# Performance work log

Measured on AMD Instinct MI355X. Metric: run time of the kernel, lower is better.

Reference implementation:

```python
import jax, jax.numpy as jnp
import numpy as np
from jax import lax

B, CIN, H, W = 2, 512, 64, 64
CD = CIN // 2            # down_dim = 256
CQ = CD // 8             # q/k channels = 32
EPS = 1e-5               # BatchNorm eps


def _conv3(x, w, b):
    # 3x3 conv, stride 1, padding 1 (init padding=1), NCHW/OIHW
    y = lax.conv_general_dilated(x, w, (1, 1), [(1, 1), (1, 1)],
                                 dimension_numbers=('NCHW', 'OIHW', 'NCHW'))
    return y + b[None, :, None, None]


def _bn(x, g, b, m, v):
    scale = g / jnp.sqrt(v + EPS)
    return x * scale[None, :, None, None] + (b - m * scale)[None, :, None, None]


def _prelu(x, a):
    return jnp.where(x > 0, x, a * x)


def _p1(x, w, b):
    # 1x1 conv as channel matmul
    return jnp.einsum('bchw,oc->bohw', x, w) + b[None, :, None, None]


def setup_inputs() -> dict:
    key = jax.random.key(0)
    it = iter(jax.random.split(key, 64))
    def nrm(shape, s=0.05):
        return jax.random.normal(next(it), shape, jnp.float32) * s
    inp = {
        'input_rgb': jax.random.normal(next(it), (B, CIN, H, W), jnp.float32),
        'input_dsm': jax.random.normal(next(it), (B, CIN, H, W), jnp.float32),
    }
    for m in ('rgb', 'dsm'):
        inp['conv_w_' + m] = nrm((CD, CIN, 3, 3))
        inp['conv_b_' + m] = nrm((CD,))
        inp['bn_g_' + m] = 1.0 + nrm((CD,))
        inp['bn_b_' + m] = nrm((CD,))
        inp['bn_m_' + m] = nrm((CD,))
        inp['bn_v_' + m] = jax.random.uniform(next(it), (CD,), jnp.float32, 0.5, 1.5)
        inp['prelu_' + m] = jnp.float32(0.25)
        inp['q_w_' + m] = nrm((CQ, CD)); inp['q_b_' + m] = nrm((CQ,))
        inp['k_w_' + m] = nrm((CQ, CD)); inp['k_b_' + m] = nrm((CQ,))
        inp['v_w_' + m] = nrm((CD, CD)); inp['v_b_' + m] = nrm((CD,))
        inp['up_w_' + m] = nrm((CIN, CD)); inp['up_b_' + m] = nrm((CIN,))
        inp['gamma_' + m] = jnp.float32(0.1)  # learned residual gate (zero-init in torch)
    return inp


def reference(input_rgb, input_dsm,
              conv_w_rgb, conv_b_rgb, bn_g_rgb, bn_b_rgb, bn_m_rgb, bn_v_rgb, prelu_rgb,
              q_w_rgb, q_b_rgb, k_w_rgb, k_b_rgb, v_w_rgb, v_b_rgb, up_w_rgb, up_b_rgb, gamma_rgb,
              conv_w_dsm, conv_b_dsm, bn_g_dsm, bn_b_dsm, bn_m_dsm, bn_v_dsm, prelu_dsm,
              q_w_dsm, q_b_dsm, k_w_dsm, k_b_dsm, v_w_dsm, v_b_dsm, up_w_dsm, up_b_dsm, gamma_dsm):
    conv_rgb = _prelu(_bn(_conv3(input_rgb, conv_w_rgb, conv_b_rgb),
                          bn_g_rgb, bn_b_rgb, bn_m_rgb, bn_v_rgb), prelu_rgb)
    conv_dsm = _prelu(_bn(_conv3(input_dsm, conv_w_dsm, conv_b_dsm),
                          bn_g_dsm, bn_b_dsm, bn_m_dsm, bn_v_dsm), prelu_dsm)
    b, c, h, w = conv_rgb.shape
    n = h * w
    q_rgb = _p1(conv_rgb, q_w_rgb, q_b_rgb).reshape(b, CQ, n)
    k_rgb = _p1(conv_rgb, k_w_rgb, k_b_rgb).reshape(b, CQ, n)
    v_rgb = _p1(conv_rgb, v_w_rgb, v_b_rgb).reshape(b, c, n)
    q_dsm = _p1(conv_dsm, q_w_dsm, q_b_dsm).reshape(b, CQ, n)
    k_dsm = _p1(conv_dsm, k_w_dsm, k_b_dsm).reshape(b, CQ, n)
    v_dsm = _p1(conv_dsm, v_w_dsm, v_b_dsm).reshape(b, c, n)
    # cross-modal unscaled attention: dsm queries attend over rgb keys
    attn_rgb = jax.nn.softmax(jnp.einsum('bqn,bqm->bnm', q_dsm, k_rgb), axis=-1)  # [b,n,n]
    o_rgb = jnp.einsum('bcj,bij->bci', v_rgb, attn_rgb).reshape(b, c, h, w)
    o_rgb = gamma_rgb * o_rgb + conv_rgb
    attn_dsm = jax.nn.softmax(jnp.einsum('bqn,bqm->bnm', q_rgb, k_dsm), axis=-1)
    o_dsm = jnp.einsum('bcj,bij->bci', v_dsm, attn_dsm).reshape(b, c, h, w)
    o_dsm = gamma_dsm * o_dsm + conv_dsm
    out_rgb = _p1(o_rgb, up_w_rgb, up_b_rgb) + input_rgb
    out_dsm = _p1(o_dsm, up_w_dsm, up_b_dsm) + input_dsm
    return (out_rgb, out_dsm)
```

## Files before the change

### kernel.cpp

```cpp
#include <hip/hip_runtime.h>
#include <hip/hip_bf16.h>
#include <stdint.h>


constexpr int CINCH = 512;
constexpr int NPIX  = 4096;

typedef __bf16 bf16x8 __attribute__((ext_vector_type(8)));
typedef __bf16 bf16x4 __attribute__((ext_vector_type(4)));
typedef float  f32x4  __attribute__((ext_vector_type(4)));

__device__ __forceinline__ __bf16 f2b(float f) {
    __hip_bfloat16 h = __float2bfloat16(f);
    return *reinterpret_cast<__bf16*>(&h);
}

__device__ __forceinline__ void load_lds16(const void* g, void* l) {
    __builtin_amdgcn_global_load_lds(
        (const __attribute__((address_space(1))) unsigned int*)(uintptr_t)g,
        (__attribute__((address_space(3))) unsigned int*)(uintptr_t)l,
        16, 0, 0);
}

__global__ __launch_bounds__(256)
void prep_w(const float* __restrict__ w_r, const float* __restrict__ w_d,
            const float* __restrict__ cb_r, const float* __restrict__ bg_r,
            const float* __restrict__ bb_r, const float* __restrict__ bm_r,
            const float* __restrict__ bv_r,
            const float* __restrict__ cb_d, const float* __restrict__ bg_d,
            const float* __restrict__ bb_d, const float* __restrict__ bm_d,
            const float* __restrict__ bv_d,
            __bf16* __restrict__ Wt, float* __restrict__ scA,
            float* __restrict__ shB, __bf16* __restrict__ zrow)
{
    const int t = threadIdx.x;
    const int blk = blockIdx.x;
    if (blk < 2304) {
        int gid = blk * 1024 + t * 4;
        int mod = gid >= 1179648;
        int o2  = gid - mod * 1179648;
        int tap = o2 >> 17;
        int r   = o2 & 131071;
        int oc  = r >> 9;
        int ic  = r & 511;
        const float* wsrc = mod ? w_d : w_r;
        long base = ((long)(oc * 512 + ic)) * 9 + tap;
        bf16x4 v;
        v.x = f2b(wsrc[base]);
        v.y = f2b(wsrc[base + 9]);
        v.z = f2b(wsrc[base + 18]);
        v.w = f2b(wsrc[base + 27]);
        *(bf16x4*)&Wt[gid] = v;
    } else if (blk == 2304) {
        unsigned short* z = (unsigned short*)zrow;
        z[t] = 0; z[t + 256] = 0;
    } else {
        int mod = blk - 2305;
        const float* cb = mod ? cb_d : cb_r;
        const float* bg = mod ? bg_d : bg_r;
        const float* bb = mod ? bb_d : bb_r;
        const float* bm = mod ? bm_d : bm_r;
        const float* bv = mod ? bv_d : bv_r;
        int oc = t;
        float sc = bg[oc] * rsqrtf(bv[oc] + 1e-5f);
        scA[mod * 256 + oc] = sc;
        shB[mod * 256 + oc] = (cb[oc] - bm[oc]) * sc + bb[oc];
    }
}

__global__ __launch_bounds__(256)
void prep_gw(const float* __restrict__ qw_r, const float* __restrict__ qw_d,
             const float* __restrict__ kw_r, const float* __restrict__ kw_d,
             const float* __restrict__ vw_r, const float* __restrict__ vw_d,
             const float* __restrict__ uw_r, const float* __restrict__ uw_d,
             __bf16* __restrict__ Wq, __bf16* __restrict__ Wk,
             __bf16* __restrict__ Wv, __bf16* __restrict__ Wu)
{
    int gid = blockIdx.x * 1024 + threadIdx.x * 4;
    __bf16* dst;
    float4 f = make_float4(0.f, 0.f, 0.f, 0.f);
    if (gid < 65536) {
        int mod = gid >> 15, e = gid & 32767;
        dst = Wq + gid;
        if (e < 8192) f = *(const float4*)((mod ? qw_d : qw_r) + e);
    } else if (gid < 131072) {
        int g = gid - 65536;
        int mod = g >> 15, e = g & 32767;
        dst = Wk + g;
        if (e < 8192) f = *(const float4*)((mod ? kw_d : kw_r) + e);
    } else if (gid < 262144) {
        int g = gid - 131072;
        int mod = g >> 16, e = g & 65535;
        dst = Wv + g;
        f = *(const float4*)((mod ? vw_d : vw_r) + e);
    } else {
        int g = gid - 262144;
        int mod = g >> 17, e = g & 131071;
        dst = Wu + g;
        f = *(const float4*)((mod ? uw_d : uw_r) + e);
    }
    bf16x4 o; o.x = f2b(f.x); o.y = f2b(f.y); o.z = f2b(f.z); o.w = f2b(f.w);
    *(bf16x4*)dst = o;
}

__global__ __launch_bounds__(256)
void xpose(const float* __restrict__ inr, const float* __restrict__ ind,
           __bf16* __restrict__ Xp)
{
    __shared__ float tile[32][33];
    const int t = threadIdx.x;
    const int p0 = blockIdx.x * 32;
    const int ic0 = blockIdx.y * 32;
    const int mb = blockIdx.z;
    const int mod = mb >> 1, b = mb & 1;
    const float* src = (mod ? ind : inr) + (long)b * CINCH * NPIX;

    int i = t >> 3, j4 = (t & 7) * 4;
    float4 v = *(const float4*)&src[(long)(ic0 + i) * NPIX + p0 + j4];
    tile[i][j4 + 0] = v.x; tile[i][j4 + 1] = v.y;
    tile[i][j4 + 2] = v.z; tile[i][j4 + 3] = v.w;
    __syncthreads();
    int j = t >> 3, i4 = (t & 7) * 4;
    bf16x4 o;
    o.x = f2b(tile[i4 + 0][j]);
    o.y = f2b(tile[i4 + 1][j]);
    o.z = f2b(tile[i4 + 2][j]);
    o.w = f2b(tile[i4 + 3][j]);
    *(bf16x4*)&Xp[((long)mb * NPIX + p0 + j) * 512 + ic0 + i4] = o;
}

__global__ __launch_bounds__(256)
void t256(const float* __restrict__ src, __bf16* __restrict__ dst)
{
    __shared__ float tile[32][33];
    const int t = threadIdx.x;
    const int p0 = blockIdx.x * 32;
    const int c0 = blockIdx.y * 32;
    const int mb = blockIdx.z;
    const float* s = src + (long)mb * 256 * NPIX;
    __bf16* d = dst + (long)mb * NPIX * 256;

    int i = t >> 3, j4 = (t & 7) * 4;
    float4 v = *(const float4*)&s[(long)(c0 + i) * NPIX + p0 + j4];
    tile[i][j4 + 0] = v.x; tile[i][j4 + 1] = v.y;
    tile[i][j4 + 2] = v.z; tile[i][j4 + 3] = v.w;
    __syncthreads();
    int j = t >> 3, i4 = (t & 7) * 4;
    bf16x4 o;
    o.x = f2b(tile[i4 + 0][j]); o.y = f2b(tile[i4 + 1][j]);
    o.z = f2b(tile[i4 + 2][j]); o.w = f2b(tile[i4 + 3][j]);
    *(bf16x4*)&d[((long)(p0 + j)) * 256 + c0 + i4] = o;
}

__global__ __launch_bounds__(256)
void conv_mfma(const __bf16* __restrict__ Wt, const __bf16* __restrict__ Xp,
               const __bf16* __restrict__ zrow, const float* __restrict__ scA,
               const float* __restrict__ shB, const float* __restrict__ prr,
               const float* __restrict__ prd, float* __restrict__ conv)
{
    __shared__ __bf16 As[64 * 32];
    __shared__ __bf16 Bs[128 * 32];

    const int t = threadIdx.x;
    const int n0 = blockIdx.x * 128;
    const int m0 = blockIdx.y * 64;
    const int mb = blockIdx.z;
    const int mod = mb >> 1;

    const __bf16* Am = Wt + (long)mod * 9 * 256 * 512;
    const __bf16* Xb = Xp + (long)mb * NPIX * 512;

    const int rowa = t >> 2;
    const int c16  = t & 3;
    char* ldsA  = (char*)As + (t >> 6) * 1024;
    char* ldsB0 = (char*)Bs + (t >> 6) * 1024;
    char* ldsB1 = ldsB0 + 4096;

    const int lane = t & 63, quad = lane >> 4, l15 = lane & 15, w = t >> 6;
    const int nw0 = w * 32;
    const char* abase = (const char*)As + l15 * 64 + quad * 16;
    const char* bbase = (const char*)Bs + (nw0 + l15) * 64 + quad * 16;

    f32x4 acc[4][2];
#pragma unroll
    for (int i = 0; i < 4; ++i)
#pragma unroll
        for (int j = 0; j < 2; ++j) acc[i][j] = (f32x4)0.f;

    for (int tap = 0; tap < 9; ++tap) {
        const int dy = tap / 3 - 1, dx = tap % 3 - 1;
        const __bf16* srcA = Am + (long)tap * 131072 + (long)(m0 + rowa) * 512 + c16 * 8;
        const __bf16* srcB0; const __bf16* srcB1;
        bool v0, v1;
        {
            int n = n0 + rowa;
            int x = n & 63, y = n >> 6;
            v0 = !((dx == -1 && x == 0) || (dx == 1 && x == 63) ||
                   (dy == -1 && y == 0) || (dy == 1 && y == 63));
            srcB0 = v0 ? (Xb + (long)(n + dy * 64 + dx) * 512 + c16 * 8)
                       : (zrow + c16 * 8);
            n += 64; x = n & 63; y = n >> 6;
            v1 = !((dx == -1 && x == 0) || (dx == 1 && x == 63) ||
                   (dy == -1 && y == 0) || (dy == 1 && y == 63));
            srcB1 = v1 ? (Xb + (long)(n + dy * 64 + dx) * 512 + c16 * 8)
                       : (zrow + c16 * 8);
        }

        for (int ic0 = 0; ic0 < 512; ic0 += 32) {
            load_lds16(srcA + ic0, ldsA);
            load_lds16(srcB0 + (v0 ? ic0 : 0), ldsB0);
            load_lds16(srcB1 + (v1 ? ic0 : 0), ldsB1);
            __syncthreads();

            bf16x8 af[4], bfr[2];
#pragma unroll
            for (int i = 0; i < 4; ++i) af[i]  = *(const bf16x8*)(abase + i * 1024);
#pragma unroll
            for (int j = 0; j < 2; ++j) bfr[j] = *(const bf16x8*)(bbase + j * 1024);
#pragma unroll
            for (int i = 0; i < 4; ++i)
#pragma unroll
                for (int j = 0; j < 2; ++j)
                    acc[i][j] = __builtin_amdgcn_mfma_f32_16x16x32_bf16(
                        af[i], bfr[j], acc[i][j], 0, 0, 0);
            __syncthreads();
        }
    }

    const float alpha = (mod ? prd : prr)[0];
    float* outp = conv + (long)mb * 256 * NPIX;
#pragma unroll
    for (int i = 0; i < 4; ++i) {
#pragma unroll
        for (int r = 0; r < 4; ++r) {
            int oc = m0 + 16 * i + quad * 4 + r;
            float sc = scA[mod * 256 + oc];
            float sh = shB[mod * 256 + oc];
            float* orow = outp + (long)oc * NPIX;
#pragma unroll
            for (int j = 0; j < 2; ++j) {
                int n = n0 + nw0 + 16 * j + l15;
                float y = acc[i][j][r] * sc + sh;
                y = (y > 0.f) ? y : alpha * y;
                orow[n] = y;
            }
        }
    }
}

__global__ __launch_bounds__(256)
void proj_mfma(const __bf16* __restrict__ Wb, int mstride,
               const __bf16* __restrict__ Bt,
               const float* __restrict__ bias_r, const float* __restrict__ bias_d,
               __bf16* __restrict__ dstT, __bf16* __restrict__ dstV,
               float* __restrict__ dstU,
               const float* __restrict__ resid_r, const float* __restrict__ resid_d,
               int mode)
{
    __shared__ __bf16 As[128 * 32];
    __shared__ __bf16 Bs[128 * 32];

    const int t = threadIdx.x;
    const int n0 = blockIdx.x * 128;
    const int m0 = blockIdx.y * 128;
    const int mb = blockIdx.z;
    const int mod = mb >> 1, b = mb & 1;

    const __bf16* Am = Wb + (long)mod * mstride;
    const __bf16* Bm = Bt + (long)mb * (NPIX * 256);
    const float* bias = mod ? bias_d : bias_r;

    const int rowa = t >> 2, c16 = t & 3;
    char* ldsA0 = (char*)As + (t >> 6) * 1024;
    char* ldsA1 = ldsA0 + 4096;
    char* ldsB0 = (char*)Bs + (t >> 6) * 1024;
    char* ldsB1 = ldsB0 + 4096;
    const __bf16* srcA = Am + (long)(m0 + rowa) * 256 + c16 * 8;
    const __bf16* srcB = Bm + (long)(n0 + rowa) * 256 + c16 * 8;

    const int lane = t & 63, quad = lane >> 4, l15 = lane & 15, w = t >> 6;
    const int mw = (w >> 1) * 64, nw = (w & 1) * 64;
    const char* abase = (const char*)As + (mw + l15) * 64 + quad * 16;
    const char* bbase = (const char*)Bs + (nw + l15) * 64 + quad * 16;

    f32x4 acc[4][4];
#pragma unroll
    for (int i = 0; i < 4; ++i)
#pragma unroll
        for (int j = 0; j < 4; ++j) acc[i][j] = (f32x4)0.f;

    for (int kc = 0; kc < 256; kc += 32) {
        load_lds16(srcA + kc, ldsA0);
        load_lds16(srcA + kc + 16384, ldsA1);
        load_lds16(srcB + kc, ldsB0);
        load_lds16(srcB + kc + 16384, ldsB1);
        __syncthreads();

        bf16x8 af[4], bfr[4];
#pragma unroll
        for (int i = 0; i < 4; ++i) af[i]  = *(const bf16x8*)(abase + i * 1024);
#pragma unroll
        for (int j = 0; j < 4; ++j) bfr[j] = *(const bf16x8*)(bbase + j * 1024);
#pragma unroll
        for (int i = 0; i < 4; ++i)
#pragma unroll
            for (int j = 0; j < 4; ++j)
                acc[i][j] = __builtin_amdgcn_mfma_f32_16x16x32_bf16(
                    af[i], bfr[j], acc[i][j], 0, 0, 0);
        __syncthreads();
    }

    if (mode == 0) {
        if (mw == 0) {
            __bf16* dbase = dstT + (long)mb * (NPIX * 32);
#pragma unroll
            for (int fi = 0; fi < 2; ++fi)
#pragma unroll
                for (int r = 0; r < 4; ++r) {
                    int oc = 16 * fi + quad * 4 + r;
                    float bi = bias[oc];
#pragma unroll
                    for (int fj = 0; fj < 4; ++fj) {
                        int n = n0 + nw + 16 * fj + l15;
                        dbase[(long)n * 32 + oc] = f2b(acc[fi][fj][r] + bi);
                    }
                }
        }
    } else if (mode == 1) {
        __bf16* dv = dstV + (long)mb * (256 * NPIX);
#pragma unroll
        for (int fi = 0; fi < 4; ++fi)
#pragma unroll
            for (int r = 0; r < 4; ++r) {
                int c = m0 + mw + 16 * fi + quad * 4 + r;
                float bi = bias[c];
                __bf16* row = dv + (long)c * NPIX;
#pragma unroll
                for (int fj = 0; fj < 4; ++fj) {
                    int n = n0 + nw + 16 * fj + l15;
                    row[n] = f2b(acc[fi][fj][r] + bi);
                }
            }
    } else {
        float* du = dstU + (long)mod * 4194304 + (long)b * 2097152;
        const float* rs = (mod ? resid_d : resid_r) + (long)b * 2097152;
#pragma unroll
        for (int fi = 0; fi < 4; ++fi)
#pragma unroll
            for (int r = 0; r < 4; ++r) {
                int oc = m0 + mw + 16 * fi + quad * 4 + r;
                float bi = bias[oc];
                const float* rrow = rs + (long)oc * NPIX;
                float* orow = du + (long)oc * NPIX;
#pragma unroll
                for (int fj = 0; fj < 4; ++fj) {
                    int n = n0 + nw + 16 * fj + l15;
                    orow[n] = acc[fi][fj][r] + bi + rrow[n];
                }
            }
    }
}

__global__ __launch_bounds__(256)
void attn_stats_mfma(const __bf16* __restrict__ Qt, const __bf16* __restrict__ Kt,
                     float* __restrict__ rmp, float* __restrict__ rlp)
{
    __shared__ __bf16 Qs[128 * 32];
    __shared__ __bf16 Ks[128 * 32];
    __shared__ float red[2][128];
    __shared__ float mfin[128];

    const int t  = threadIdx.x;
    const int i0 = blockIdx.x * 128;
    const int mbo = blockIdx.y;
    const int o  = mbo >> 1, b = mbo & 1;
    const int seg = blockIdx.z;
    const int jbase = seg * 2048;
    const int mbK = o * 2 + b, mbQ = (1 - o) * 2 + b;

    const __bf16* Qg = Qt + (long)mbQ * 131072;
    const __bf16* Kg = Kt + (long)mbK * 131072;

    const int lane = t & 63, quad = lane >> 4, l15 = lane & 15, w = t >> 6;
    const int mS = (w >> 1) * 64;
    const int nS = (w & 1) * 64;

    load_lds16((const char*)Qg + (long)i0 * 64 + t * 16, (char*)Qs + (t >> 6) * 1024);
    load_lds16((const char*)Qg + (long)i0 * 64 + 4096 + t * 16,
               (char*)Qs + 4096 + (t >> 6) * 1024);
    __syncthreads();

    bf16x8 qa[4];
#pragma unroll
    for (int fi = 0; fi < 4; ++fi)
        qa[fi] = *(const bf16x8*)((const char*)Qs + (mS + 16 * fi + l15) * 64 + quad * 16);

    const f32x4 zero4 = (f32x4)0.f;
    float mloc[16];
#pragma unroll
    for (int e = 0; e < 16; ++e) mloc[e] = -3.0e38f;

    for (int j0 = jbase; j0 < jbase + 2048; j0 += 128) {
        __syncthreads();
        load_lds16((const char*)Kg + (long)j0 * 64 + t * 16, (char*)Ks + (t >> 6) * 1024);
        load_lds16((const char*)Kg + (long)j0 * 64 + 4096 + t * 16,
                   (char*)Ks + 4096 + (t >> 6) * 1024);
        __syncthreads();
#pragma unroll
        for (int fj = 0; fj < 4; ++fj) {
            bf16x8 kb = *(const bf16x8*)((const char*)Ks + (nS + 16 * fj + l15) * 64 + quad * 16);
#pragma unroll
            for (int fi = 0; fi < 4; ++fi) {
                f32x4 s = __builtin_amdgcn_mfma_f32_16x16x32_bf16(qa[fi], kb, zero4, 0, 0, 0);
#pragma unroll
                for (int r = 0; r < 4; ++r)
                    mloc[fi * 4 + r] = fmaxf(mloc[fi * 4 + r], s[r]);
            }
        }
    }
#pragma unroll
    for (int d = 1; d < 16; d <<= 1)
#pragma unroll
        for (int e = 0; e < 16; ++e)
            mloc[e] = fmaxf(mloc[e], __shfl_xor(mloc[e], d, 64));
    if (l15 == 0) {
#pragma unroll
        for (int fi = 0; fi < 4; ++fi)
#pragma unroll
            for (int r = 0; r < 4; ++r)
                red[w & 1][mS + 16 * fi + quad * 4 + r] = mloc[fi * 4 + r];
    }
    __syncthreads();
    if (t < 128) mfin[t] = fmaxf(red[0][t], red[1][t]);
    __syncthreads();

    float mi[16];
#pragma unroll
    for (int fi = 0; fi < 4; ++fi)
#pragma unroll
        for (int r = 0; r < 4; ++r)
            mi[fi * 4 + r] = mfin[mS + 16 * fi + quad * 4 + r];
    float sloc[16];
#pragma unroll
    for (int e = 0; e < 16; ++e) sloc[e] = 0.f;

    for (int j0 = jbase; j0 < jbase + 2048; j0 += 128) {
        __syncthreads();
        load_lds16((const char*)Kg + (long)j0 * 64 + t * 16, (char*)Ks + (t >> 6) * 1024);
        load_lds16((const char*)Kg + (long)j0 * 64 + 4096 + t * 16,
                   (char*)Ks + 4096 + (t >> 6) * 1024);
        __syncthreads();
#pragma unroll
        for (int fj = 0; fj < 4; ++fj) {
            bf16x8 kb = *(const bf16x8*)((const char*)Ks + (nS + 16 * fj + l15) * 64 + quad * 16);
#pragma unroll
            for (int fi = 0; fi < 4; ++fi) {
                f32x4 s = __builtin_amdgcn_mfma_f32_16x16x32_bf16(qa[fi], kb, zero4, 0, 0, 0);
#pragma unroll
                for (int r = 0; r < 4; ++r)
                    sloc[fi * 4 + r] += __expf(s[r] - mi[fi * 4 + r]);
            }
        }
    }
#pragma unroll
    for (int d = 1; d < 16; d <<= 1)
#pragma unroll
        for (int e = 0; e < 16; ++e)
            sloc[e] += __shfl_xor(sloc[e], d, 64);
    if (l15 == 0) {
#pragma unroll
        for (int fi = 0; fi < 4; ++fi)
#pragma unroll
            for (int r = 0; r < 4; ++r)
                red[w & 1][mS + 16 * fi + quad * 4 + r] = sloc[fi * 4 + r];
    }
    __syncthreads();
    if (t < 128) {
        rmp[seg * 16384 + mbo * 4096 + i0 + t] = mfin[t];
        rlp[seg * 16384 + mbo * 4096 + i0 + t] = red[0][t] + red[1][t];
    }
}

__global__ __launch_bounds__(256)
void stats_merge(const float* __restrict__ rmp, const float* __restrict__ rlp,
                 float* __restrict__ rmb, float* __restrict__ rlb)
{
    int idx = blockIdx.x * 256 + threadIdx.x;
    float m0 = rmp[idx], m1 = rmp[16384 + idx];
    float l0 = rlp[idx], l1 = rlp[16384 + idx];
    float m = fmaxf(m0, m1);
    float l = l0 * __expf(m0 - m) + l1 * __expf(m1 - m);
    rmb[idx] = m;
    rlb[idx] = 1.f / l;
}

__global__ __launch_bounds__(256)
void attn_pv_mfma(const __bf16* __restrict__ Qt, const __bf16* __restrict__ Kt,
                  const __bf16* __restrict__ Vb,
                  float* __restrict__ part0, float* __restrict__ part1,
                  const float* __restrict__ rmb, const float* __restrict__ rlb)
{
    __shared__ __bf16 Qs[128 * 32];
    __shared__ __bf16 Ks[64 * 32];
    __shared__ __bf16 Vs[2 * 128 * 32];
    __shared__ __bf16 Ps[2 * 128 * 32];

    const int t  = threadIdx.x;
    const int i0 = blockIdx.x * 128;
    const int c0 = blockIdx.y * 128;
    const int zb = blockIdx.z;
    const int seg = zb >> 2, mb = zb & 3;
    const int o  = mb >> 1, b = mb & 1;
    const int mbK = mb, mbQ = (1 - o) * 2 + b;
    const int jbase = seg * 2048;

    const __bf16* Qg = Qt + (long)mbQ * 131072;
    const __bf16* Kg = Kt + (long)mbK * 131072;
    const __bf16* Vg = Vb + (long)mbK * 1048576;
    const float* rm = rmb + mb * 4096;
    const float* rl = rlb + mb * 4096;

    const int lane = t & 63, quad = lane >> 4, l15 = lane & 15, w = t >> 6;
    const int mw = (w >> 1) * 64;
    const int nw = (w & 1) * 64;
    const int mS = (w >> 1) * 64;
    const int nS = (w & 1) * 32;
    const int ksP = w & 1;

    load_lds16((const char*)Qg + (long)i0 * 64 + t * 16, (char*)Qs + (t >> 6) * 1024);
    load_lds16((const char*)Qg + (long)i0 * 64 + 4096 + t * 16,
               (char*)Qs + 4096 + (t >> 6) * 1024);

    float mlv[16], rlv[16];
#pragma unroll
    for (int fi = 0; fi < 4; ++fi)
#pragma unroll
        for (int r = 0; r < 4; ++r) {
            int i = i0 + mS + 16 * fi + quad * 4 + r;
            mlv[fi * 4 + r] = rm[i];
            rlv[fi * 4 + r] = rl[i];
        }

    f32x4 acc[4][4];
#pragma unroll
    for (int i = 0; i < 4; ++i)
#pragma unroll
        for (int j = 0; j < 4; ++j) acc[i][j] = (f32x4)0.f;
    const f32x4 zero4 = (f32x4)0.f;

    for (int j0 = jbase; j0 < jbase + 2048; j0 += 64) {
        __syncthreads();
        load_lds16((const char*)Kg + (long)j0 * 64 + t * 16, (char*)Ks + (t >> 6) * 1024);
#pragma unroll
        for (int ii = 0; ii < 4; ++ii) {
            int s = ii * 256 + t;
            int ks = s >> 9, cc = (s >> 2) & 127, blk = s & 3;
            load_lds16((const char*)Vg + (long)(c0 + cc) * 8192 + (j0 + ks * 32) * 2 + blk * 16,
                       (char*)Vs + ii * 4096 + (t >> 6) * 1024);
        }
        __syncthreads();

        bf16x8 qa[4], kb2[2];
#pragma unroll
        for (int fi = 0; fi < 4; ++fi)
            qa[fi] = *(const bf16x8*)((const char*)Qs + (mS + 16 * fi + l15) * 64 + quad * 16);
#pragma unroll
        for (int fj = 0; fj < 2; ++fj)
            kb2[fj] = *(const bf16x8*)((const char*)Ks + (nS + 16 * fj + l15) * 64 + quad * 16);
        f32x4 sA[4][2];
#pragma unroll
        for (int fi = 0; fi < 4; ++fi)
#pragma unroll
            for (int fj = 0; fj < 2; ++fj)
                sA[fi][fj] = __builtin_amdgcn_mfma_f32_16x16x32_bf16(
                    qa[fi], kb2[fj], zero4, 0, 0, 0);

        __bf16* prow = Ps + ksP * 4096;
#pragma unroll
        for (int fi = 0; fi < 4; ++fi)
#pragma unroll
            for (int fj = 0; fj < 2; ++fj) {
                int jl = 16 * fj + l15;
#pragma unroll
                for (int r = 0; r < 4; ++r) {
                    float p = __expf(sA[fi][fj][r] - mlv[fi * 4 + r]) * rlv[fi * 4 + r];
                    prow[(mS + 16 * fi + quad * 4 + r) * 32 + jl] = f2b(p);
                }
            }
        __syncthreads();

#pragma unroll
        for (int ks = 0; ks < 2; ++ks) {
            bf16x8 va[4], pb[4];
#pragma unroll
            for (int fi = 0; fi < 4; ++fi)
                va[fi] = *(const bf16x8*)((const char*)Vs + ks * 8192 +
                                          (mw + 16 * fi + l15) * 64 + quad * 16);
#pragma unroll
            for (int fj = 0; fj < 4; ++fj)
                pb[fj] = *(const bf16x8*)((const char*)Ps + ks * 8192 +
                                          (nw + 16 * fj + l15) * 64 + quad * 16);
#pragma unroll
            for (int fi = 0; fi < 4; ++fi)
#pragma unroll
                for (int fj = 0; fj < 4; ++fj)
                    acc[fi][fj] = __builtin_amdgcn_mfma_f32_16x16x32_bf16(
                        va[fi], pb[fj], acc[fi][fj], 0, 0, 0);
        }
    }

    float* pg = (seg ? part1 : part0) + (long)mb * 1048576;
#pragma unroll
    for (int fi = 0; fi < 4; ++fi) {
#pragma unroll
        for (int r = 0; r < 4; ++r) {
            int c = c0 + mw + 16 * fi + quad * 4 + r;
            float* zr = pg + (long)c * 4096;
#pragma unroll
            for (int fj = 0; fj < 4; ++fj) {
                int i = i0 + nw + 16 * fj + l15;
                zr[i] = acc[fi][fj][r];
            }
        }
    }
}

__global__ __launch_bounds__(256)
void zred_t(const float* __restrict__ p0, const float* __restrict__ p1,
            const float* __restrict__ convb, __bf16* __restrict__ Zt,
            const float* __restrict__ g_r, const float* __restrict__ g_d)
{
    __shared__ float tile[32][33];
    const int t = threadIdx.x;
    const int pix0 = blockIdx.x * 32;
    const int c0 = blockIdx.y * 32;
    const int mb = blockIdx.z;
    const int o = mb >> 1;
    const float gamma = (o ? g_d : g_r)[0];
    const long base = (long)mb * 1048576;

    int i = t >> 3, j4 = (t & 7) * 4;
    long row = base + (long)(c0 + i) * 4096 + pix0 + j4;
    float4 a = *(const float4*)&p0[row];
    float4 b = *(const float4*)&p1[row];
    float4 cv = *(const float4*)&convb[row];
    tile[i][j4 + 0] = gamma * (a.x + b.x) + cv.x;
    tile[i][j4 + 1] = gamma * (a.y + b.y) + cv.y;
    tile[i][j4 + 2] = gamma * (a.z + b.z) + cv.z;
    tile[i][j4 + 3] = gamma * (a.w + b.w) + cv.w;
    __syncthreads();
    int j = t >> 3, i4 = (t & 7) * 4;
    bf16x4 oq;
    oq.x = f2b(tile[i4 + 0][j]); oq.y = f2b(tile[i4 + 1][j]);
    oq.z = f2b(tile[i4 + 2][j]); oq.w = f2b(tile[i4 + 3][j]);
    *(bf16x4*)&Zt[(long)mb * NPIX * 256 + (long)(pix0 + j) * 256 + c0 + i4] = oq;
}

extern "C" void kernel_launch(void* const* d_in, const int* in_sizes, int n_in,
                              void* d_out, int out_size, void* d_ws, size_t ws_size,
                              hipStream_t stream)
{
    const float* in_rgb = (const float*)d_in[0];
    const float* in_dsm = (const float*)d_in[1];
    auto P = [&](int i) { return (const float*)d_in[i]; };

    float* ws    = (float*)d_ws;
    float* conv  = ws;
    float* part0 = ws + 4194304;
    float* rmb   = ws + 8388608;
    float* rlb   = ws + 8404992;
    float* rmp   = ws + 8421376;
    float* rlp   = ws + 8454144;
    float* scA   = ws + 8486912;
    float* shB   = ws + 8487424;
    __bf16* zrow = (__bf16*)(ws + 8487936);
    __bf16* Wt   = (__bf16*)(ws + 8488192);
    __bf16* Xp   = (__bf16*)(ws + 9667840);
    float*  part1 = ws + 9667840;
    __bf16* Qt   = (__bf16*)(ws + 13862144);
    __bf16* Kt   = (__bf16*)(ws + 14124288);
    __bf16* Vbb  = (__bf16*)(ws + 14386432);
    __bf16* Ct   = (__bf16*)(ws + 16483584);
    __bf16* Zt   = (__bf16*)(ws + 18580736);
    __bf16* Wq   = (__bf16*)(ws + 20677888);
    __bf16* Wk   = (__bf16*)(ws + 20710656);
    __bf16* Wv   = (__bf16*)(ws + 20743424);
    __bf16* Wu   = (__bf16*)(ws + 20808960);

    prep_w<<<2307, 256, 0, stream>>>(
        P(2), P(18), P(3), P(4), P(5), P(6), P(7),
        P(19), P(20), P(21), P(22), P(23),
        Wt, scA, shB, zrow);
    prep_gw<<<512, 256, 0, stream>>>(
        P(9), P(25), P(11), P(27), P(13), P(29), P(15), P(31),
        Wq, Wk, Wv, Wu);
    xpose<<<dim3(128, 16, 4), 256, 0, stream>>>(in_rgb, in_dsm, Xp);

    conv_mfma<<<dim3(32, 4, 4), 256, 0, stream>>>(
        Wt, Xp, zrow, scA, shB, P(8), P(24), conv);
    t256<<<dim3(128, 8, 4), 256, 0, stream>>>(conv, Ct);

    proj_mfma<<<dim3(32, 1, 4), 256, 0, stream>>>(
        Wq, 32768, Ct, P(10), P(26), Qt, nullptr, nullptr, nullptr, nullptr, 0);
    proj_mfma<<<dim3(32, 1, 4), 256, 0, stream>>>(
        Wk, 32768, Ct, P(12), P(28), Kt, nullptr, nullptr, nullptr, nullptr, 0);
    proj_mfma<<<dim3(32, 2, 4), 256, 0, stream>>>(
        Wv, 65536, Ct, P(14), P(30), nullptr, Vbb, nullptr, nullptr, nullptr, 1);

    attn_stats_mfma<<<dim3(32, 4, 2), 256, 0, stream>>>(Qt, Kt, rmp, rlp);
    stats_merge<<<64, 256, 0, stream>>>(rmp, rlp, rmb, rlb);

    attn_pv_mfma<<<dim3(32, 2, 8), 256, 0, stream>>>(
        Qt, Kt, Vbb, part0, part1, rmb, rlb);

    zred_t<<<dim3(128, 8, 4), 256, 0, stream>>>(
        part0, part1, conv, Zt, P(17), P(33));

    proj_mfma<<<dim3(32, 4, 4), 256, 0, stream>>>(
        Wu, 131072, Zt, P(16), P(32), nullptr, nullptr, (float*)d_out,
        in_rgb, in_dsm, 2);
}
```

Before: 406.0 us.

## Use online softmax stats, exp2 prescaling, and retile attention PV over all channels

Queries are prescaled by log2(e) so every exponential becomes exp2f. The softmax-stats kernel now computes the running max and sum in one pass with online rescaling instead of two passes over K, and it splits keys into four segments that are merged afterwards. The PV kernel now covers all 256 channels per block with 64 query rows, so QK^T and the exponentials are computed once per row rather than once per channel half. It also uses an XOR-swizzled P tile and applies the 1/l normalization at the output. The trade-offs are more exp work per element in the online pass, more registers and LDS for V, and reuse of the part0 buffer for the stats scratch.

```diff
diff --git a/kernel.cpp b/kernel.cpp
--- a/kernel.cpp
+++ b/kernel.cpp
@@ -255,7 +255,7 @@
                __bf16* __restrict__ dstT, __bf16* __restrict__ dstV,
                float* __restrict__ dstU,
                const float* __restrict__ resid_r, const float* __restrict__ resid_d,
-               int mode)
+               int mode, float oscale)
 {
     __shared__ __bf16 As[128 * 32];
     __shared__ __bf16 Bs[128 * 32];
@@ -322,7 +322,7 @@
 #pragma unroll
                     for (int fj = 0; fj < 4; ++fj) {
                         int n = n0 + nw + 16 * fj + l15;
-                        dbase[(long)n * 32 + oc] = f2b(acc[fi][fj][r] + bi);
+                        dbase[(long)n * 32 + oc] = f2b((acc[fi][fj][r] + bi) * oscale);
                     }
                 }
         }
@@ -367,15 +367,15 @@
 {
     __shared__ __bf16 Qs[128 * 32];
     __shared__ __bf16 Ks[128 * 32];
-    __shared__ float red[2][128];
-    __shared__ float mfin[128];
+    __shared__ float redm[2][128];
+    __shared__ float redl[2][128];
 
     const int t  = threadIdx.x;
     const int i0 = blockIdx.x * 128;
     const int mbo = blockIdx.y;
     const int o  = mbo >> 1, b = mbo & 1;
     const int seg = blockIdx.z;
-    const int jbase = seg * 2048;
+    const int jbase = seg * 1024;
     const int mbK = o * 2 + b, mbQ = (1 - o) * 2 + b;
 
     const __bf16* Qg = Qt + (long)mbQ * 131072;
@@ -385,9 +385,9 @@
     const int mS = (w >> 1) * 64;
     const int nS = (w & 1) * 64;
 
-    load_lds16((const char*)Qg + (long)i0 * 64 + t * 16, (char*)Qs + (t >> 6) * 1024);
+    load_lds16((const char*)Qg + (long)i0 * 64 + t * 16, (char*)Qs + w * 1024);
     load_lds16((const char*)Qg + (long)i0 * 64 + 4096 + t * 16,
-               (char*)Qs + 4096 + (t >> 6) * 1024);
+               (char*)Qs + 4096 + w * 1024);
     __syncthreads();
 
     bf16x8 qa[4];
@@ -396,88 +396,67 @@
         qa[fi] = *(const bf16x8*)((const char*)Qs + (mS + 16 * fi + l15) * 64 + quad * 16);
 
     const f32x4 zero4 = (f32x4)0.f;
-    float mloc[16];
-#pragma unroll
-    for (int e = 0; e < 16; ++e) mloc[e] = -3.0e38f;
-
-    for (int j0 = jbase; j0 < jbase + 2048; j0 += 128) {
+    float m_t[16], l_t[16];
+#pragma unroll
+    for (int e = 0; e < 16; ++e) { m_t[e] = -3.0e38f; l_t[e] = 0.f; }
+
+    for (int j0 = jbase; j0 < jbase + 1024; j0 += 128) {
         __syncthreads();
-        load_lds16((const char*)Kg + (long)j0 * 64 + t * 16, (char*)Ks + (t >> 6) * 1024);
+        load_lds16((const char*)Kg + (long)j0 * 64 + t * 16, (char*)Ks + w * 1024);
         load_lds16((const char*)Kg + (long)j0 * 64 + 4096 + t * 16,
-                   (char*)Ks + 4096 + (t >> 6) * 1024);
+                   (char*)Ks + 4096 + w * 1024);
         __syncthreads();
-#pragma unroll
-        for (int fj = 0; fj < 4; ++fj) {
-            bf16x8 kb = *(const bf16x8*)((const char*)Ks + (nS + 16 * fj + l15) * 64 + quad * 16);
-#pragma unroll
-            for (int fi = 0; fi < 4; ++fi) {
-                f32x4 s = __builtin_amdgcn_mfma_f32_16x16x32_bf16(qa[fi], kb, zero4, 0, 0, 0);
-#pragma unroll
-                for (int r = 0; r < 4; ++r)
-                    mloc[fi * 4 + r] = fmaxf(mloc[fi * 4 + r], s[r]);
+
+        bf16x8 kb[4];
+#pragma unroll
+        for (int fj = 0; fj < 4; ++fj)
+            kb[fj] = *(const bf16x8*)((const char*)Ks + (nS + 16 * fj + l15) * 64 + quad * 16);
+#pragma unroll
+        for (int fi = 0; fi < 4; ++fi) {
+            f32x4 sf[4];
+#pragma unroll
+            for (int fj = 0; fj < 4; ++fj)
+                sf[fj] = __builtin_amdgcn_mfma_f32_16x16x32_bf16(qa[fi], kb[fj], zero4, 0, 0, 0);
+#pragma unroll
+            for (int r = 0; r < 4; ++r) {
+                int e = fi * 4 + r;
+                float a = fmaxf(fmaxf(sf[0][r], sf[1][r]), fmaxf(sf[2][r], sf[3][r]));
+                float nm = fmaxf(m_t[e], a);
+                float s = exp2f(sf[0][r] - nm) + exp2f(sf[1][r] - nm)
+                        + exp2f(sf[2][r] - nm) + exp2f(sf[3][r] - nm);
+                l_t[e] = l_t[e] * exp2f(m_t[e] - nm) + s;
+                m_t[e] = nm;
             }
         }
     }
+
 #pragma unroll
     for (int d = 1; d < 16; d <<= 1)
 #pragma unroll
-        for (int e = 0; e < 16; ++e)
-            mloc[e] = fmaxf(mloc[e], __shfl_xor(mloc[e], d, 64));
+        for (int e = 0; e < 16; ++e) {
+            float om = __shfl_xor(m_t[e], d, 64);
+            float ol = __shfl_xor(l_t[e], d, 64);
+            float nm = fmaxf(m_t[e], om);
+            l_t[e] = l_t[e] * exp2f(m_t[e] - nm) + ol * exp2f(om - nm);
+            m_t[e] = nm;
+        }
     if (l15 == 0) {
 #pragma unroll
         for (int fi = 0; fi < 4; ++fi)
 #pragma unroll
-            for (int r = 0; r < 4; ++r)
-                red[w & 1][mS + 16 * fi + quad * 4 + r] = mloc[fi * 4 + r];
-    }
-    __syncthreads();
-    if (t < 128) mfin[t] = fmaxf(red[0][t], red[1][t]);
-    __syncthreads();
-
-    float mi[16];
-#pragma unroll
-    for (int fi = 0; fi < 4; ++fi)
-#pragma unroll
-        for (int r = 0; r < 4; ++r)
-            mi[fi * 4 + r] = mfin[mS + 16 * fi + quad * 4 + r];
-    float sloc[16];
-#pragma unroll
-    for (int e = 0; e < 16; ++e) sloc[e] = 0.f;
-
-    for (int j0 = jbase; j0 < jbase + 2048; j0 += 128) {
-        __syncthreads();
-        load_lds16((const char*)Kg + (long)j0 * 64 + t * 16, (char*)Ks + (t >> 6) * 1024);
-        load_lds16((const char*)Kg + (long)j0 * 64 + 4096 + t * 16,
-                   (char*)Ks + 4096 + (t >> 6) * 1024);
-        __syncthreads();
-#pragma unroll
-        for (int fj = 0; fj < 4; ++fj) {
-            bf16x8 kb = *(const bf16x8*)((const char*)Ks + (nS + 16 * fj + l15) * 64 + quad * 16);
-#pragma unroll
-            for (int fi = 0; fi < 4; ++fi) {
-                f32x4 s = __builtin_amdgcn_mfma_f32_16x16x32_bf16(qa[fi], kb, zero4, 0, 0, 0);
-#pragma unroll
-                for (int r = 0; r < 4; ++r)
-                    sloc[fi * 4 + r] += __expf(s[r] - mi[fi * 4 + r]);
+            for (int r = 0; r < 4; ++r) {
+                redm[w & 1][mS + 16 * fi + quad * 4 + r] = m_t[fi * 4 + r];
+                redl[w & 1][mS + 16 * fi + quad * 4 + r] = l_t[fi * 4 + r];
             }
-        }
-    }
-#pragma unroll
-    for (int d = 1; d < 16; d <<= 1)
-#pragma unroll
-        for (int e = 0; e < 16; ++e)
-            sloc[e] += __shfl_xor(sloc[e], d, 64);
-    if (l15 == 0) {
-#pragma unroll
-        for (int fi = 0; fi < 4; ++fi)
-#pragma unroll
-            for (int r = 0; r < 4; ++r)
-                red[w & 1][mS + 16 * fi + quad * 4 + r] = sloc[fi * 4 + r];
     }
     __syncthreads();
     if (t < 128) {
-        rmp[seg * 16384 + mbo * 4096 + i0 + t] = mfin[t];
-        rlp[seg * 16384 + mbo * 4096 + i0 + t] = red[0][t] + red[1][t];
+        float m0 = redm[0][t], m1 = redm[1][t];
+        float l0 = redl[0][t], l1 = redl[1][t];
+        float m = fmaxf(m0, m1);
+        float l = l0 * exp2f(m0 - m) + l1 * exp2f(m1 - m);
+        rmp[seg * 16384 + mbo * 4096 + i0 + t] = m;
+        rlp[seg * 16384 + mbo * 4096 + i0 + t] = l;
     }
 }
 
@@ -486,10 +465,13 @@
                  float* __restrict__ rmb, float* __restrict__ rlb)
 {
     int idx = blockIdx.x * 256 + threadIdx.x;
-    float m0 = rmp[idx], m1 = rmp[16384 + idx];
-    float l0 = rlp[idx], l1 = rlp[16384 + idx];
-    float m = fmaxf(m0, m1);
-    float l = l0 * __expf(m0 - m) + l1 * __expf(m1 - m);
+    float m = rmp[idx];
+#pragma unroll
+    for (int s = 1; s < 4; ++s) m = fmaxf(m, rmp[s * 16384 + idx]);
+    float l = 0.f;
+#pragma unroll
+    for (int s = 0; s < 4; ++s)
+        l += rlp[s * 16384 + idx] * exp2f(rmp[s * 16384 + idx] - m);
     rmb[idx] = m;
     rlb[idx] = 1.f / l;
 }
@@ -500,16 +482,15 @@
                   float* __restrict__ part0, float* __restrict__ part1,
                   const float* __restrict__ rmb, const float* __restrict__ rlb)
 {
-    __shared__ __bf16 Qs[128 * 32];
+    __shared__ __bf16 Qs[64 * 32];
     __shared__ __bf16 Ks[64 * 32];
-    __shared__ __bf16 Vs[2 * 128 * 32];
-    __shared__ __bf16 Ps[2 * 128 * 32];
+    __shared__ __bf16 Vs[2 * 256 * 32];
+    __shared__ __bf16 Ps[64 * 64];
 
     const int t  = threadIdx.x;
-    const int i0 = blockIdx.x * 128;
-    const int c0 = blockIdx.y * 128;
-    const int zb = blockIdx.z;
-    const int seg = zb >> 2, mb = zb & 3;
+    const int i0 = blockIdx.x * 64;
+    const int seg = blockIdx.y;
+    const int mb = blockIdx.z;
     const int o  = mb >> 1, b = mb & 1;
     const int mbK = mb, mbQ = (1 - o) * 2 + b;
     const int jbase = seg * 2048;
@@ -521,25 +502,16 @@
     const float* rl = rlb + mb * 4096;
 
     const int lane = t & 63, quad = lane >> 4, l15 = lane & 15, w = t >> 6;
-    const int mw = (w >> 1) * 64;
-    const int nw = (w & 1) * 64;
-    const int mS = (w >> 1) * 64;
-    const int nS = (w & 1) * 32;
-    const int ksP = w & 1;
-
-    load_lds16((const char*)Qg + (long)i0 * 64 + t * 16, (char*)Qs + (t >> 6) * 1024);
-    load_lds16((const char*)Qg + (long)i0 * 64 + 4096 + t * 16,
-               (char*)Qs + 4096 + (t >> 6) * 1024);
-
-    float mlv[16], rlv[16];
-#pragma unroll
-    for (int fi = 0; fi < 4; ++fi)
-#pragma unroll
-        for (int r = 0; r < 4; ++r) {
-            int i = i0 + mS + 16 * fi + quad * 4 + r;
-            mlv[fi * 4 + r] = rm[i];
-            rlv[fi * 4 + r] = rl[i];
-        }
+    const int iS = w * 16;
+    const int cw = w * 64;
+
+    load_lds16((const char*)Qg + (long)i0 * 64 + t * 16, (char*)Qs + w * 1024);
+
+    float mlv[4], rlv[4];
+#pragma unroll
+    for (int r = 0; r < 4; ++r) mlv[r] = rm[i0 + iS + quad * 4 + r];
+#pragma unroll
+    for (int fj = 0; fj < 4; ++fj) rlv[fj] = rl[i0 + 16 * fj + l15];
 
     f32x4 acc[4][4];
 #pragma unroll
@@ -548,44 +520,38 @@
         for (int j = 0; j < 4; ++j) acc[i][j] = (f32x4)0.f;
     const f32x4 zero4 = (f32x4)0.f;
 
+    __syncthreads();
+    const bf16x8 qa = *(const bf16x8*)((const char*)Qs + (iS + l15) * 64 + quad * 16);
+
+    const int clv = w * 16 + (lane >> 2);
+    const int jb8 = (lane & 3) * 8;
+
     for (int j0 = jbase; j0 < jbase + 2048; j0 += 64) {
         __syncthreads();
-        load_lds16((const char*)Kg + (long)j0 * 64 + t * 16, (char*)Ks + (t >> 6) * 1024);
-#pragma unroll
-        for (int ii = 0; ii < 4; ++ii) {
-            int s = ii * 256 + t;
-            int ks = s >> 9, cc = (s >> 2) & 127, blk = s & 3;
-            load_lds16((const char*)Vg + (long)(c0 + cc) * 8192 + (j0 + ks * 32) * 2 + blk * 16,
-                       (char*)Vs + ii * 4096 + (t >> 6) * 1024);
-        }
+        load_lds16((const char*)Kg + (long)j0 * 64 + t * 16, (char*)Ks + w * 1024);
         __syncthreads();
 
-        bf16x8 qa[4], kb2[2];
-#pragma unroll
-        for (int fi = 0; fi < 4; ++fi)
-            qa[fi] = *(const bf16x8*)((const char*)Qs + (mS + 16 * fi + l15) * 64 + quad * 16);
-#pragma unroll
-        for (int fj = 0; fj < 2; ++fj)
-            kb2[fj] = *(const bf16x8*)((const char*)Ks + (nS + 16 * fj + l15) * 64 + quad * 16);
-        f32x4 sA[4][2];
-#pragma unroll
-        for (int fi = 0; fi < 4; ++fi)
-#pragma unroll
-            for (int fj = 0; fj < 2; ++fj)
-                sA[fi][fj] = __builtin_amdgcn_mfma_f32_16x16x32_bf16(
-                    qa[fi], kb2[fj], zero4, 0, 0, 0);
-
-        __bf16* prow = Ps + ksP * 4096;
-#pragma unroll
-        for (int fi = 0; fi < 4; ++fi)
-#pragma unroll
-            for (int fj = 0; fj < 2; ++fj) {
-                int jl = 16 * fj + l15;
-#pragma unroll
-                for (int r = 0; r < 4; ++r) {
-                    float p = __expf(sA[fi][fj][r] - mlv[fi * 4 + r]) * rlv[fi * 4 + r];
-                    prow[(mS + 16 * fi + quad * 4 + r) * 32 + jl] = f2b(p);
-                }
+#pragma unroll
+        for (int ii = 0; ii < 8; ++ii) {
+            int ks = ii >> 2;
+            int c = (ii & 3) * 64 + clv;
+            load_lds16((const char*)Vg + (long)c * 8192 + (long)(j0 + ks * 32 + jb8) * 2,
+                       (char*)Vs + ii * 4096 + w * 1024);
+        }
+
+        f32x4 sA[4];
+#pragma unroll
+        for (int fj = 0; fj < 4; ++fj) {
+            bf16x8 kb = *(const bf16x8*)((const char*)Ks + (16 * fj + l15) * 64 + quad * 16);
+            sA[fj] = __builtin_amdgcn_mfma_f32_16x16x32_bf16(qa, kb, zero4, 0, 0, 0);
+        }
+#pragma unroll
+        for (int fj = 0; fj < 4; ++fj)
+#pragma unroll
+            for (int r = 0; r < 4; ++r) {
+                int il = iS + quad * 4 + r;
+                int boff = (il * 128 + (16 * fj + l15) * 2) ^ ((il & 12) << 3);
+                *(__bf16*)((char*)Ps + boff) = f2b(exp2f(sA[fj][r] - mlv[r]));
             }
         __syncthreads();
 
@@ -594,12 +560,14 @@
             bf16x8 va[4], pb[4];
 #pragma unroll
             for (int fi = 0; fi < 4; ++fi)
-                va[fi] = *(const bf16x8*)((const char*)Vs + ks * 8192 +
-                                          (mw + 16 * fi + l15) * 64 + quad * 16);
-#pragma unroll
-            for (int fj = 0; fj < 4; ++fj)
-                pb[fj] = *(const bf16x8*)((const char*)Ps + ks * 8192 +
-                                          (nw + 16 * fj + l15) * 64 + quad * 16);
+                va[fi] = *(const bf16x8*)((const char*)Vs + ks * 16384 +
+                                          (cw + 16 * fi + l15) * 64 + quad * 16);
+#pragma unroll
+            for (int fj = 0; fj < 4; ++fj) {
+                int ip = 16 * fj + l15;
+                int boff = (ip * 128 + ks * 64 + quad * 16) ^ ((ip & 12) << 3);
+                pb[fj] = *(const bf16x8*)((const char*)Ps + boff);
+            }
 #pragma unroll
             for (int fi = 0; fi < 4; ++fi)
 #pragma unroll
@@ -614,13 +582,11 @@
     for (int fi = 0; fi < 4; ++fi) {
 #pragma unroll
         for (int r = 0; r < 4; ++r) {
-            int c = c0 + mw + 16 * fi + quad * 4 + r;
+            int c = cw + 16 * fi + quad * 4 + r;
             float* zr = pg + (long)c * 4096;
 #pragma unroll
-            for (int fj = 0; fj < 4; ++fj) {
-                int i = i0 + nw + 16 * fj + l15;
-                zr[i] = acc[fi][fj][r];
-            }
+            for (int fj = 0; fj < 4; ++fj)
+                zr[i0 + 16 * fj + l15] = acc[fi][fj][r] * rlv[fj];
         }
     }
 }
@@ -669,8 +635,8 @@
     float* part0 = ws + 4194304;
     float* rmb   = ws + 8388608;
     float* rlb   = ws + 8404992;
-    float* rmp   = ws + 8421376;
-    float* rlp   = ws + 8454144;
+    float* rmp   = part0;
+    float* rlp   = part0 + 65536;
     float* scA   = ws + 8486912;
     float* shB   = ws + 8487424;
     __bf16* zrow = (__bf16*)(ws + 8487936);
@@ -701,16 +667,19 @@
     t256<<<dim3(128, 8, 4), 256, 0, stream>>>(conv, Ct);
 
     proj_mfma<<<dim3(32, 1, 4), 256, 0, stream>>>(
-        Wq, 32768, Ct, P(10), P(26), Qt, nullptr, nullptr, nullptr, nullptr, 0);
+        Wq, 32768, Ct, P(10), P(26), Qt, nullptr, nullptr, nullptr, nullptr,
+        0, 1.4426950408889634f);
     proj_mfma<<<dim3(32, 1, 4), 256, 0, stream>>>(
-        Wk, 32768, Ct, P(12), P(28), Kt, nullptr, nullptr, nullptr, nullptr, 0);
+        Wk, 32768, Ct, P(12), P(28), Kt, nullptr, nullptr, nullptr, nullptr,
+        0, 1.0f);
     proj_mfma<<<dim3(32, 2, 4), 256, 0, stream>>>(
-        Wv, 65536, Ct, P(14), P(30), nullptr, Vbb, nullptr, nullptr, nullptr, 1);
-
-    attn_stats_mfma<<<dim3(32, 4, 2), 256, 0, stream>>>(Qt, Kt, rmp, rlp);
+        Wv, 65536, Ct, P(14), P(30), nullptr, Vbb, nullptr, nullptr, nullptr,
+        1, 1.0f);
+
+    attn_stats_mfma<<<dim3(32, 4, 4), 256, 0, stream>>>(Qt, Kt, rmp, rlp);
     stats_merge<<<64, 256, 0, stream>>>(rmp, rlp, rmb, rlb);
 
-    attn_pv_mfma<<<dim3(32, 2, 8), 256, 0, stream>>>(
+    attn_pv_mfma<<<dim3(64, 2, 4), 256, 0, stream>>>(
         Qt, Kt, Vbb, part0, part1, rmb, rlb);
 
     zred_t<<<dim3(128, 8, 4), 256, 0, stream>>>(
@@ -718,5 +687,5 @@
 
     proj_mfma<<<dim3(32, 4, 4), 256, 0, stream>>>(
         Wu, 131072, Zt, P(16), P(32), nullptr, nullptr, (float*)d_out,
-        in_rgb, in_dsm, 2);
-}
+        in_rgb, in_dsm, 2, 1.0f);
+}
```

After: 385.9 us. 1.05x faster.
